# Kernel optimization log

Hardware: AMD Instinct MI355X
Metric: run time of the kernel (lower is better)

## Reference

```python
import jax, jax.numpy as jnp
import numpy as np

NY, NX, C = 496, 432, 64
B = 4
N_PER = 12000  # pillars per sample


def setup_inputs() -> dict:
    key = jax.random.key(0)
    N = B * N_PER
    voxel_features = jax.random.normal(key, (N, C), dtype=jnp.float32)
    # Build coords with unique (y, x) cells per batch sample (as real voxelization produces).
    rng = np.random.default_rng(0)
    coords_np = np.zeros((N, 4), dtype=np.int32)
    for b in range(B):
        flat = rng.choice(NY * NX, size=N_PER, replace=False)
        s = slice(b * N_PER, (b + 1) * N_PER)
        coords_np[s, 0] = b
        coords_np[s, 2] = flat // NX
        coords_np[s, 3] = flat % NX
    return {
        "voxel_features": voxel_features,
        "coords": jnp.asarray(coords_np),
        "batch_size": B,
    }


def reference(voxel_features, coords, batch_size):
    # Global flat index: b * (ny*nx) + y * nx + x  -> single fused scatter.
    idx = (coords[:, 0].astype(jnp.int32) * (NY * NX)
           + coords[:, 2].astype(jnp.int32) * NX
           + coords[:, 3].astype(jnp.int32))
    canvas = jnp.zeros((batch_size * NY * NX, C), dtype=voxel_features.dtype)
    canvas = canvas.at[idx].set(voxel_features)
    # [B*ny*nx, C] -> [B, C, ny, nx]
    return canvas.reshape(batch_size, NY, NX, C).transpose(0, 3, 1, 2)
```

## Files before the change

### kernel.cpp

```cpp
#include <hip/hip_runtime.h>
#include <stdint.h>

#define NYv 496
#define NXv 432
#define Cv  64
#define Bv  4
#define PLANE (NYv * NXv)
#define NVEC (NXv / 4)
#define RPB 2
#define ACTIVE (RPB * NVEC)
#define CSPLIT 4
#define CCHUNK (Cv / CSPLIT)

#define OFF_R ((size_t)(3 * Cv + 60) * PLANE)

__global__ __launch_bounds__(256) void scatter_idx(const int4* __restrict__ coords,
                                                   int* __restrict__ outw, int n) {
    int i = blockIdx.x * 256 + threadIdx.x;
    if (i >= n) return;
    int4 c4 = coords[i];
    outw[OFF_R + (size_t)c4.x * PLANE + c4.z * NXv + c4.w] = i;
}

__device__ __forceinline__ float4 pack4(const float* __restrict__ feats,
                                        const int* p, int c) {
    float4 f;
    f.x = (p[0] >= 0) ? feats[(size_t)p[0] * Cv + c] : 0.0f;
    f.y = (p[1] >= 0) ? feats[(size_t)p[1] * Cv + c] : 0.0f;
    f.z = (p[2] >= 0) ? feats[(size_t)p[2] * Cv + c] : 0.0f;
    f.w = (p[3] >= 0) ? feats[(size_t)p[3] * Cv + c] : 0.0f;
    return f;
}

__global__ __launch_bounds__(256) void gather_main(const float* __restrict__ feats,
                                                   float* __restrict__ out) {
    int lane = (int)threadIdx.x;
    if (lane >= ACTIVE) return;
    int r = lane / NVEC;
    int v = lane - r * NVEC;
    int g = blockIdx.x * RPB + r;
    int b = g / NYv;
    int y = g - b * NYv;
    int c0 = blockIdx.y * CCHUNK;

    const int* cnv = (const int*)out + OFF_R + (size_t)b * PLANE + y * NXv + v * 4;
    int4 pi = *reinterpret_cast<const int4*>(cnv);
    int p[4] = {pi.x, pi.y, pi.z, pi.w};

    float* outp = out + ((size_t)(b * Cv + c0)) * PLANE + y * NXv + v * 4;
    for (int c = 0; c < CCHUNK; ++c) {
        if (b == 3 && c0 + c >= 60) break;
        *reinterpret_cast<float4*>(outp + (size_t)c * PLANE) = pack4(feats, p, c0 + c);
    }
}

__global__ __launch_bounds__(256) void gather_tail3(const float* __restrict__ feats,
                                                    float* __restrict__ out) {
    int lane = (int)threadIdx.x;
    if (lane >= ACTIVE) return;
    int r = lane / NVEC;
    int v = lane - r * NVEC;
    int y = blockIdx.x * RPB + r;
    int j = blockIdx.y;

    const int* cnv = (const int*)out + OFF_R + (size_t)3 * PLANE + y * NXv + v * 4;
    int4 pi = *reinterpret_cast<const int4*>(cnv);
    int p[4] = {pi.x, pi.y, pi.z, pi.w};

    float* outp = out + OFF_R + (size_t)j * PLANE + y * NXv + v * 4;
    *reinterpret_cast<float4*>(outp) = pack4(feats, p, 60 + j);
}

__global__ __launch_bounds__(256) void gather_tail_last(const float* __restrict__ feats,
                                                        float* __restrict__ out) {
    int lane = (int)threadIdx.x;
    if (lane >= ACTIVE) return;
    int r = lane / NVEC;
    int v = lane - r * NVEC;
    int y = blockIdx.x * RPB + r;

    float* cellf = out + OFF_R + (size_t)3 * PLANE + y * NXv + v * 4;
    int4 pi = *reinterpret_cast<const int4*>(cellf);
    int p[4] = {pi.x, pi.y, pi.z, pi.w};
    *reinterpret_cast<float4*>(cellf) = pack4(feats, p, 63);
}

extern "C" void kernel_launch(void* const* d_in, const int* in_sizes, int n_in,
                              void* d_out, int out_size, void* d_ws, size_t ws_size,
                              hipStream_t stream) {
    const float* feats  = (const float*)d_in[0];
    const int*   coords = (const int*)d_in[1];
    int n = in_sizes[0] / Cv;
    float* out = (float*)d_out;
    int*   outw = (int*)d_out;

    hipMemsetAsync(outw + OFF_R, 0xFF, (size_t)Bv * PLANE * sizeof(int), stream);

    scatter_idx<<<(n + 255) / 256, 256, 0, stream>>>((const int4*)coords, outw, n);

    dim3 gmain((Bv * NYv) / RPB, CSPLIT);
    gather_main<<<gmain, 256, 0, stream>>>(feats, out);

    dim3 gtail(NYv / RPB, 3);
    gather_tail3<<<gtail, 256, 0, stream>>>(feats, out);

    gather_tail_last<<<NYv / RPB, 256, 0, stream>>>(feats, out);
}
```

Baseline: 233.6 us.

## Move index canvas to workspace and collapse tail kernels into one gather

The index canvas moves from the tail of the output buffer into the separate workspace buffer. Because nothing aliases any more, the two tail kernels that handled channels 60-63 of the last batch sample are dropped and a single gather kernel writes all channels. The gather loop also gets an unroll pragma. This removes two extra launches and the serialized tail passes, but it relies on the workspace being large enough to hold the canvas.

```diff
diff --git a/kernel.cpp b/kernel.cpp
--- a/kernel.cpp
+++ b/kernel.cpp
@@ -12,14 +12,12 @@
 #define CSPLIT 4
 #define CCHUNK (Cv / CSPLIT)
 
-#define OFF_R ((size_t)(3 * Cv + 60) * PLANE)
-
 __global__ __launch_bounds__(256) void scatter_idx(const int4* __restrict__ coords,
-                                                   int* __restrict__ outw, int n) {
+                                                   int* __restrict__ canvas, int n) {
     int i = blockIdx.x * 256 + threadIdx.x;
     if (i >= n) return;
     int4 c4 = coords[i];
-    outw[OFF_R + (size_t)c4.x * PLANE + c4.z * NXv + c4.w] = i;
+    canvas[((size_t)c4.x * NYv + c4.z) * NXv + c4.w] = i;
 }
 
 __device__ __forceinline__ float4 pack4(const float* __restrict__ feats,
@@ -32,8 +30,9 @@
     return f;
 }
 
-__global__ __launch_bounds__(256) void gather_main(const float* __restrict__ feats,
-                                                   float* __restrict__ out) {
+__global__ __launch_bounds__(256) void gather_all(const float* __restrict__ feats,
+                                                  const int* __restrict__ canvas,
+                                                  float* __restrict__ out) {
     int lane = (int)threadIdx.x;
     if (lane >= ACTIVE) return;
     int r = lane / NVEC;
@@ -43,46 +42,14 @@
     int y = g - b * NYv;
     int c0 = blockIdx.y * CCHUNK;
 
-    const int* cnv = (const int*)out + OFF_R + (size_t)b * PLANE + y * NXv + v * 4;
-    int4 pi = *reinterpret_cast<const int4*>(cnv);
+    int4 pi = *reinterpret_cast<const int4*>(canvas + (size_t)g * NXv + v * 4);
     int p[4] = {pi.x, pi.y, pi.z, pi.w};
 
     float* outp = out + ((size_t)(b * Cv + c0)) * PLANE + y * NXv + v * 4;
+#pragma unroll 4
     for (int c = 0; c < CCHUNK; ++c) {
-        if (b == 3 && c0 + c >= 60) break;
         *reinterpret_cast<float4*>(outp + (size_t)c * PLANE) = pack4(feats, p, c0 + c);
     }
-}
-
-__global__ __launch_bounds__(256) void gather_tail3(const float* __restrict__ feats,
-                                                    float* __restrict__ out) {
-    int lane = (int)threadIdx.x;
-    if (lane >= ACTIVE) return;
-    int r = lane / NVEC;
-    int v = lane - r * NVEC;
-    int y = blockIdx.x * RPB + r;
-    int j = blockIdx.y;
-
-    const int* cnv = (const int*)out + OFF_R + (size_t)3 * PLANE + y * NXv + v * 4;
-    int4 pi = *reinterpret_cast<const int4*>(cnv);
-    int p[4] = {pi.x, pi.y, pi.z, pi.w};
-
-    float* outp = out + OFF_R + (size_t)j * PLANE + y * NXv + v * 4;
-    *reinterpret_cast<float4*>(outp) = pack4(feats, p, 60 + j);
-}
-
-__global__ __launch_bounds__(256) void gather_tail_last(const float* __restrict__ feats,
-                                                        float* __restrict__ out) {
-    int lane = (int)threadIdx.x;
-    if (lane >= ACTIVE) return;
-    int r = lane / NVEC;
-    int v = lane - r * NVEC;
-    int y = blockIdx.x * RPB + r;
-
-    float* cellf = out + OFF_R + (size_t)3 * PLANE + y * NXv + v * 4;
-    int4 pi = *reinterpret_cast<const int4*>(cellf);
-    int p[4] = {pi.x, pi.y, pi.z, pi.w};
-    *reinterpret_cast<float4*>(cellf) = pack4(feats, p, 63);
 }
 
 extern "C" void kernel_launch(void* const* d_in, const int* in_sizes, int n_in,
@@ -91,18 +58,13 @@
     const float* feats  = (const float*)d_in[0];
     const int*   coords = (const int*)d_in[1];
     int n = in_sizes[0] / Cv;
-    float* out = (float*)d_out;
-    int*   outw = (int*)d_out;
+    float* out    = (float*)d_out;
+    int*   canvas = (int*)d_ws;
 
-    hipMemsetAsync(outw + OFF_R, 0xFF, (size_t)Bv * PLANE * sizeof(int), stream);
+    hipMemsetAsync(canvas, 0xFF, (size_t)Bv * PLANE * sizeof(int), stream);
 
-    scatter_idx<<<(n + 255) / 256, 256, 0, stream>>>((const int4*)coords, outw, n);
+    scatter_idx<<<(n + 255) / 256, 256, 0, stream>>>((const int4*)coords, canvas, n);
 
     dim3 gmain((Bv * NYv) / RPB, CSPLIT);
-    gather_main<<<gmain, 256, 0, stream>>>(feats, out);
-
-    dim3 gtail(NYv / RPB, 3);
-    gather_tail3<<<gtail, 256, 0, stream>>>(feats, out);
-
-    gather_tail_last<<<NYv / RPB, 256, 0, stream>>>(feats, out);
+    gather_all<<<gmain, 256, 0, stream>>>(feats, canvas, out);
 }
```

Measured after the change: 231.1 us. About the same (-1.1%).
